# Kernel optimization log

Measured on AMD Instinct MI355X. Metric: run time of the kernel, lower is better.

## Reference

```python
import jax, jax.numpy as jnp
import numpy as np
from jax import lax

DIM = 128
HEADS = 8
B, H, W = 8, 128, 128


def conv1x1(w, x):
    # w: [out_c, in_c], x: [b, in_c, h, w]
    return jnp.einsum('oc,bchw->bohw', w, x)


def setup_inputs() -> dict:
    key = jax.random.key(0)
    ks = jax.random.split(key, 12)
    s = 0.02
    return {
        'x': jax.random.normal(ks[0], (B, DIM, H, W), dtype=jnp.float32),
        'W_qkv': jax.random.normal(ks[1], (3 * DIM, DIM), dtype=jnp.float32) * s,
        'W_dw': jax.random.normal(ks[2], (DIM, 1, 3, 3), dtype=jnp.float32) * s,
        'W_proj_s': jax.random.normal(ks[3], (DIM, DIM), dtype=jnp.float32) * s,
        'scale_s': jnp.ones((HEADS, 1, 1), dtype=jnp.float32),
        'W_ff1': jax.random.normal(ks[4], (DIM, DIM), dtype=jnp.float32) * s,
        'W_ff2': jax.random.normal(ks[5], (DIM, DIM), dtype=jnp.float32) * s,
        'W_proj_f': jax.random.normal(ks[6], (DIM, DIM), dtype=jnp.float32) * s,
        'W_gsf': jax.random.normal(ks[7], (DIM, DIM), dtype=jnp.float32) * s,
        'b_gsf': jnp.zeros((DIM,), dtype=jnp.float32),
        'W_gfs': jax.random.normal(ks[8], (DIM, DIM), dtype=jnp.float32) * s,
        'b_gfs': jnp.zeros((DIM,), dtype=jnp.float32),
    }


def reference(x, W_qkv, W_dw, W_proj_s, scale_s, W_ff1, W_ff2, W_proj_f,
              W_gsf, b_gsf, W_gfs, b_gfs):
    b, c, h, w = x.shape
    head = HEADS
    ch = c // head

    # --- channel self-attention branch ---
    qkv = conv1x1(W_qkv, x)                      # [b, 3c, h, w]
    q_s, k_s, v_s = jnp.split(qkv, 3, axis=1)
    v_s_conv = lax.conv_general_dilated(
        v_s, W_dw, window_strides=(1, 1), padding='SAME',
        feature_group_count=c,
        dimension_numbers=('NCHW', 'OIHW', 'NCHW'))  # depthwise 3x3

    q = q_s.reshape(b, head, ch, h * w)
    k = k_s.reshape(b, head, ch, h * w)
    v = v_s.reshape(b, head, ch, h * w)
    attn = jax.nn.softmax(jnp.einsum('bhcn,bhdn->bhcd', q, k) * scale_s, axis=-1)
    out_s = jnp.einsum('bhcd,bhdn->bhcn', attn, v).reshape(b, c, h, w)
    out_s = conv1x1(W_proj_s, out_s + v_s_conv)

    # --- frequency filter branch ---
    xf = jnp.fft.rfft2(x, norm='ortho')          # complex [b,c,h,w//2+1]
    spatial_weights = conv1x1(W_ff2, jax.nn.gelu(conv1x1(W_ff1, x), approximate=False))
    freq_weights = jnp.fft.rfft2(spatial_weights, norm='ortho')
    out_f = jnp.fft.irfft2(xf * freq_weights, s=(h, w), norm='ortho')
    out_f = conv1x1(W_proj_f, out_f)

    # --- sigmoid-gated fusion ---
    gate_f = jax.nn.sigmoid(conv1x1(W_gsf, out_s) + b_gsf[:, None, None])
    gate_s = jax.nn.sigmoid(conv1x1(W_gfs, out_f) + b_gfs[:, None, None])
    return x + out_s * gate_s + out_f * gate_f
```

## Files before the change

kernel.cpp:

```cpp
#include <hip/hip_runtime.h>
#include <math.h>

#define HW 16384

typedef __attribute__((ext_vector_type(8))) short bf16x8;
typedef __attribute__((ext_vector_type(4))) float f32x4;

__device__ __forceinline__ unsigned f2bf_pk(float a, float b)
{
    unsigned ua = __float_as_uint(a), ub = __float_as_uint(b);
    ua = (ua + 0x7FFFu + ((ua >> 16) & 1u)) >> 16;
    ub = (ub + 0x7FFFu + ((ub >> 16) & 1u)) >> 16;
    return (ua & 0xFFFFu) | (ub << 16);
}
__device__ __forceinline__ unsigned short f2bf(float a)
{
    unsigned ua = __float_as_uint(a);
    ua = (ua + 0x7FFFu + ((ua >> 16) & 1u)) >> 16;
    return (unsigned short)ua;
}
__device__ __forceinline__ float bf2f(unsigned short u)
{
    return __uint_as_float(((unsigned)u) << 16);
}
__device__ __forceinline__ float sigmoidf_(float v) { return 1.f / (1.f + expf(-v)); }

__device__ __forceinline__ float2 cmul(float2 a, float2 b)
{
    return make_float2(a.x * b.x - a.y * b.y, a.x * b.y + a.y * b.x);
}

__device__ __forceinline__ int SWZ2(int r, int j)
{
    return j ^ (r & 7) ^ ((((j >> 4) ^ (r >> 1)) & 1) << 3);
}

__global__ __launch_bounds__(256)
void wprep_k(const float* __restrict__ w0, const float* __restrict__ w1,
             const float* __restrict__ w2, const float* __restrict__ w3,
             const float* __restrict__ w4, const float* __restrict__ w5,
             const float* __restrict__ w6, int4* __restrict__ Wbf4)
{
    int m = blockIdx.x >> 3;
    int slot = (blockIdx.x & 7) * 256 + threadIdx.x;
    const float* src;
    switch (m) {
        case 0: src = w0; break;
        case 1: src = w1; break;
        case 2: src = w2; break;
        case 3: src = w3; break;
        case 4: src = w4; break;
        case 5: src = w5; break;
        default: src = w6; break;
    }
    int o = slot >> 4;
    int c16 = (slot & 15) ^ (o & 7);
    const float* p = src + o * 128 + c16 * 8;
    int4 pk;
    pk.x = f2bf_pk(p[0], p[1]); pk.y = f2bf_pk(p[2], p[3]);
    pk.z = f2bf_pk(p[4], p[5]); pk.w = f2bf_pk(p[6], p[7]);
    Wbf4[m * 2048 + slot] = pk;
}

__global__ __launch_bounds__(256)
void conv_mfma_k(const float* __restrict__ in, const int4* __restrict__ wbf,
                 unsigned short* __restrict__ out)
{
    __shared__ short WL[128 * 128];
    __shared__ short XL[64 * 128];
    int t = threadIdx.x;
    int gb = blockIdx.x;
    int b = gb >> 8;
    int n0 = (gb & 255) << 6;

    #pragma unroll
    for (int it = 0; it < 8; ++it)
        ((int4*)WL)[it * 256 + t] = wbf[it * 256 + t];

    const float* inb = in + (size_t)b * 128 * HW + n0;
    int nl = t & 63;
    #pragma unroll
    for (int it = 0; it < 4; ++it) {
        int c8 = (t >> 6) + it * 4;
        float v[8];
        #pragma unroll
        for (int j = 0; j < 8; ++j) v[j] = inb[(size_t)(c8 * 8 + j) * HW + nl];
        int4 p;
        p.x = f2bf_pk(v[0], v[1]); p.y = f2bf_pk(v[2], v[3]);
        p.z = f2bf_pk(v[4], v[5]); p.w = f2bf_pk(v[6], v[7]);
        ((int4*)XL)[nl * 16 + (c8 ^ (nl & 7))] = p;
    }
    __syncthreads();

    int l = t & 63, w = t >> 6, kg = l >> 4, l15 = l & 15, l7 = l15 & 7;
    f32x4 acc[2][4];
    #pragma unroll
    for (int mf = 0; mf < 2; ++mf)
        #pragma unroll
        for (int nf = 0; nf < 4; ++nf) acc[mf][nf] = (f32x4){0.f, 0.f, 0.f, 0.f};
    #pragma unroll
    for (int ks = 0; ks < 4; ++ks) {
        int ch = ks * 4 + kg;
        bf16x8 A0 = ((const bf16x8*)WL)[(w * 32 + l15) * 16 + (ch ^ l7)];
        bf16x8 A1 = ((const bf16x8*)WL)[(w * 32 + 16 + l15) * 16 + (ch ^ l7)];
        #pragma unroll
        for (int nf = 0; nf < 4; ++nf) {
            bf16x8 Bf = ((const bf16x8*)XL)[(nf * 16 + l15) * 16 + (ch ^ l7)];
            acc[0][nf] = __builtin_amdgcn_mfma_f32_16x16x32_bf16(A0, Bf, acc[0][nf], 0, 0, 0);
            acc[1][nf] = __builtin_amdgcn_mfma_f32_16x16x32_bf16(A1, Bf, acc[1][nf], 0, 0, 0);
        }
    }
    #pragma unroll
    for (int mf = 0; mf < 2; ++mf)
        #pragma unroll
        for (int nf = 0; nf < 4; ++nf)
            #pragma unroll
            for (int i = 0; i < 4; ++i) {
                int row = w * 32 + mf * 16 + kg * 4 + i;
                int col = n0 + nf * 16 + l15;
                out[((size_t)b * 128 + row) * HW + col] = f2bf(acc[mf][nf][i]);
            }
}

__global__ __launch_bounds__(256)
void conv_mfma_bf_k(const unsigned short* __restrict__ in,
                    const int4* __restrict__ wbf,
                    unsigned short* __restrict__ out)
{
    __shared__ short WL[128 * 128];
    __shared__ short XL[64 * 128];
    int t = threadIdx.x;
    int gb = blockIdx.x;
    int b = gb >> 8;
    int n0 = (gb & 255) << 6;

    #pragma unroll
    for (int it = 0; it < 8; ++it)
        ((int4*)WL)[it * 256 + t] = wbf[it * 256 + t];

    const unsigned short* inb = in + (size_t)b * 128 * HW + n0;
    int nl = t & 63;
    #pragma unroll
    for (int it = 0; it < 4; ++it) {
        int c8 = (t >> 6) + it * 4;
        unsigned u[8];
        #pragma unroll
        for (int j = 0; j < 8; ++j) u[j] = inb[(size_t)(c8 * 8 + j) * HW + nl];
        int4 p;
        p.x = (int)(u[0] | (u[1] << 16)); p.y = (int)(u[2] | (u[3] << 16));
        p.z = (int)(u[4] | (u[5] << 16)); p.w = (int)(u[6] | (u[7] << 16));
        ((int4*)XL)[nl * 16 + (c8 ^ (nl & 7))] = p;
    }
    __syncthreads();

    int l = t & 63, w = t >> 6, kg = l >> 4, l15 = l & 15, l7 = l15 & 7;
    f32x4 acc[2][4];
    #pragma unroll
    for (int mf = 0; mf < 2; ++mf)
        #pragma unroll
        for (int nf = 0; nf < 4; ++nf) acc[mf][nf] = (f32x4){0.f, 0.f, 0.f, 0.f};
    #pragma unroll
    for (int ks = 0; ks < 4; ++ks) {
        int ch = ks * 4 + kg;
        bf16x8 A0 = ((const bf16x8*)WL)[(w * 32 + l15) * 16 + (ch ^ l7)];
        bf16x8 A1 = ((const bf16x8*)WL)[(w * 32 + 16 + l15) * 16 + (ch ^ l7)];
        #pragma unroll
        for (int nf = 0; nf < 4; ++nf) {
            bf16x8 Bf = ((const bf16x8*)XL)[(nf * 16 + l15) * 16 + (ch ^ l7)];
            acc[0][nf] = __builtin_amdgcn_mfma_f32_16x16x32_bf16(A0, Bf, acc[0][nf], 0, 0, 0);
            acc[1][nf] = __builtin_amdgcn_mfma_f32_16x16x32_bf16(A1, Bf, acc[1][nf], 0, 0, 0);
        }
    }
    #pragma unroll
    for (int mf = 0; mf < 2; ++mf)
        #pragma unroll
        for (int nf = 0; nf < 4; ++nf)
            #pragma unroll
            for (int i = 0; i < 4; ++i) {
                int row = w * 32 + mf * 16 + kg * 4 + i;
                int col = n0 + nf * 16 + l15;
                out[((size_t)b * 128 + row) * HW + col] = f2bf(acc[mf][nf][i]);
            }
}

__global__ __launch_bounds__(256)
void dwconv_k(const unsigned short* __restrict__ V, const float* __restrict__ Wdw,
              unsigned short* __restrict__ vcb)
{
    int tid = blockIdx.x * 256 + threadIdx.x;
    int e4 = tid & 4095;
    int bc = tid >> 12;
    int c = bc & 127;
    int y = e4 >> 5;
    int x0 = (e4 & 31) << 2;
    const unsigned short* vin = V + (size_t)bc * HW;
    float wf[9];
    #pragma unroll
    for (int i = 0; i < 9; ++i) wf[i] = Wdw[c * 9 + i];
    float a0 = 0.f, a1 = 0.f, a2 = 0.f, a3 = 0.f;
    #pragma unroll
    for (int dy = 0; dy < 3; ++dy) {
        int yy = y + dy - 1;
        if (yy < 0 || yy > 127) continue;
        const unsigned short* r = vin + yy * 128;
        uint2 mu = *(const uint2*)(r + x0);
        float m0 = bf2f((unsigned short)(mu.x & 0xFFFF));
        float m1 = bf2f((unsigned short)(mu.x >> 16));
        float m2 = bf2f((unsigned short)(mu.y & 0xFFFF));
        float m3 = bf2f((unsigned short)(mu.y >> 16));
        float left  = (x0 > 0)   ? bf2f(r[x0 - 1]) : 0.f;
        float right = (x0 < 124) ? bf2f(r[x0 + 4]) : 0.f;
        float w0 = wf[dy * 3], w1 = wf[dy * 3 + 1], w2 = wf[dy * 3 + 2];
        a0 += w0 * left + w1 * m0 + w2 * m1;
        a1 += w0 * m0   + w1 * m1 + w2 * m2;
        a2 += w0 * m1   + w1 * m2 + w2 * m3;
        a3 += w0 * m2   + w1 * m3 + w2 * right;
    }
    uint2 r2;
    r2.x = f2bf_pk(a0, a1);
    r2.y = f2bf_pk(a2, a3);
    *(uint2*)(vcb + (size_t)bc * HW + y * 128 + x0) = r2;
}

__global__ __launch_bounds__(256)
void gram_mfma_k(const float* __restrict__ x, float* __restrict__ Gp)
{
    __shared__ short XL[128 * 128];
    int t = threadIdx.x;
    int blk = blockIdx.x;
    int b = blk >> 5, ks = blk & 31;
    const float* xb = x + (size_t)b * 128 * HW + ks * 512;
    int l = t & 63, w = t >> 6, kg = l >> 4, l15 = l & 15, l7 = l15 & 7;

    f32x4 acc[2][8];
    #pragma unroll
    for (int mf = 0; mf < 2; ++mf)
        #pragma unroll
        for (int nf = 0; nf < 8; ++nf) acc[mf][nf] = (f32x4){0.f, 0.f, 0.f, 0.f};

    for (int kc = 0; kc < 4; ++kc) {
        __syncthreads();
        #pragma unroll
        for (int it = 0; it < 8; ++it) {
            int g = it * 256 + t;
            int row = g >> 4, oct = g & 15;
            const float* p = xb + (size_t)row * HW + kc * 128 + oct * 8;
            int4 pk;
            pk.x = f2bf_pk(p[0], p[1]); pk.y = f2bf_pk(p[2], p[3]);
            pk.z = f2bf_pk(p[4], p[5]); pk.w = f2bf_pk(p[6], p[7]);
            ((int4*)XL)[row * 16 + (oct ^ (row & 7))] = pk;
        }
        __syncthreads();
        #pragma unroll
        for (int s = 0; s < 4; ++s) {
            int oct = s * 4 + kg;
            bf16x8 A0 = ((const bf16x8*)XL)[(w * 32 + l15) * 16 + (oct ^ l7)];
            bf16x8 A1 = ((const bf16x8*)XL)[(w * 32 + 16 + l15) * 16 + (oct ^ l7)];
            #pragma unroll
            for (int nf = 0; nf < 8; ++nf) {
                bf16x8 Bf = ((const bf16x8*)XL)[(nf * 16 + l15) * 16 + (oct ^ l7)];
                acc[0][nf] = __builtin_amdgcn_mfma_f32_16x16x32_bf16(A0, Bf, acc[0][nf], 0, 0, 0);
                acc[1][nf] = __builtin_amdgcn_mfma_f32_16x16x32_bf16(A1, Bf, acc[1][nf], 0, 0, 0);
            }
        }
    }
    float* gp = Gp + (size_t)blk * 16384;
    #pragma unroll
    for (int mf = 0; mf < 2; ++mf)
        #pragma unroll
        for (int nf = 0; nf < 8; ++nf)
            #pragma unroll
            for (int i = 0; i < 4; ++i) {
                int row = w * 32 + mf * 16 + kg * 4 + i;
                int col = nf * 16 + l15;
                gp[row * 128 + col] = acc[mf][nf][i];
            }
}

__global__ void gram_reduce_k(const float* __restrict__ Gp, float* __restrict__ G)
{
    int idx = blockIdx.x * 256 + threadIdx.x;
    int b = idx >> 14;
    int ij = idx & 16383;
    const float* gp = Gp + (size_t)(b * 32) * 16384 + ij;
    float s = 0.f;
    #pragma unroll
    for (int ks = 0; ks < 32; ++ks) s += gp[(size_t)ks * 16384];
    G[idx] = s;
}

__global__ __launch_bounds__(256)
void attn_s2_k(const float* __restrict__ G, const float* __restrict__ Wqkv,
               const float* __restrict__ scale, float* __restrict__ S)
{
    __shared__ float Wq[16][129];
    __shared__ float Wk[16][129];
    __shared__ float Ts[16][129];
    int bh = blockIdx.x;
    int b = bh >> 3, h = bh & 7;
    int t = threadIdx.x;
    #pragma unroll
    for (int i = 0; i < 8; ++i) {
        int idx = t + i * 256;
        int r = idx >> 7, ci = idx & 127;
        Wq[r][ci] = Wqkv[(size_t)(h * 16 + r) * 128 + ci];
        Wk[r][ci] = Wqkv[(size_t)(128 + h * 16 + r) * 128 + ci];
    }
    __syncthreads();
    const float* Gb = G + (size_t)b * 16384;
    #pragma unroll
    for (int i = 0; i < 8; ++i) {
        int idx = t + i * 256;
        int c = idx >> 7, col = idx & 127;
        float s = 0.f;
        #pragma unroll 8
        for (int ci = 0; ci < 128; ++ci)
            s += Wq[c][ci] * Gb[ci * 128 + col];
        Ts[c][col] = s;
    }
    __syncthreads();
    int c = t >> 4, d = t & 15;
    float s = 0.f;
    #pragma unroll 8
    for (int col = 0; col < 128; ++col)
        s += Ts[c][col] * Wk[d][col];
    s *= scale[h];
    float m = s;
    #pragma unroll
    for (int w = 1; w < 16; w <<= 1)
        m = fmaxf(m, __shfl_xor(m, w, 64));
    float e = expf(s - m);
    float sum = e;
    #pragma unroll
    for (int w = 1; w < 16; w <<= 1)
        sum += __shfl_xor(sum, w, 64);
    S[(size_t)bh * 256 + t] = e / sum;
}

__global__ __launch_bounds__(256)
void proj_s_pv_k(const unsigned short* __restrict__ V,
                 const unsigned short* __restrict__ vcb,
                 const float* __restrict__ S, const int4* __restrict__ wbf,
                 unsigned short* __restrict__ out_s)
{
    __shared__ short WL[128 * 128];
    __shared__ short XL[64 * 128];
    __shared__ float SL[2048];
    int t = threadIdx.x;
    int gb = blockIdx.x;
    int b = gb >> 8;
    int n0 = (gb & 255) << 6;

    #pragma unroll
    for (int it = 0; it < 8; ++it)
        ((int4*)WL)[it * 256 + t] = wbf[it * 256 + t];
    #pragma unroll
    for (int i = 0; i < 8; ++i)
        SL[i * 256 + t] = S[(size_t)b * 2048 + i * 256 + t];
    __syncthreads();

    int col = t & 63, w = t >> 6;
    #pragma unroll
    for (int hh = 0; hh < 2; ++hh) {
        int h = w * 2 + hh;
        float v[16];
        #pragma unroll
        for (int d = 0; d < 16; ++d)
            v[d] = bf2f(V[((size_t)(b * 128 + h * 16 + d)) * HW + n0 + col]);
        float o[16];
        #pragma unroll
        for (int c = 0; c < 16; ++c) {
            const float* sl = SL + h * 256 + c * 16;
            float s = 0.f;
            #pragma unroll
            for (int d = 0; d < 16; ++d) s += sl[d] * v[d];
            o[c] = s + bf2f(vcb[((size_t)(b * 128 + h * 16 + c)) * HW + n0 + col]);
        }
        #pragma unroll
        for (int oc = 0; oc < 2; ++oc) {
            int octet = h * 2 + oc;
            int4 p;
            p.x = f2bf_pk(o[oc * 8 + 0], o[oc * 8 + 1]);
            p.y = f2bf_pk(o[oc * 8 + 2], o[oc * 8 + 3]);
            p.z = f2bf_pk(o[oc * 8 + 4], o[oc * 8 + 5]);
            p.w = f2bf_pk(o[oc * 8 + 6], o[oc * 8 + 7]);
            ((int4*)XL)[col * 16 + (octet ^ (col & 7))] = p;
        }
    }
    __syncthreads();

    int l = t & 63, kg = l >> 4, l15 = l & 15, l7 = l15 & 7;
    f32x4 acc[2][4];
    #pragma unroll
    for (int mf = 0; mf < 2; ++mf)
        #pragma unroll
        for (int nf = 0; nf < 4; ++nf) acc[mf][nf] = (f32x4){0.f, 0.f, 0.f, 0.f};
    #pragma unroll
    for (int ks = 0; ks < 4; ++ks) {
        int ch = ks * 4 + kg;
        bf16x8 A0 = ((const bf16x8*)WL)[(w * 32 + l15) * 16 + (ch ^ l7)];
        bf16x8 A1 = ((const bf16x8*)WL)[(w * 32 + 16 + l15) * 16 + (ch ^ l7)];
        #pragma unroll
        for (int nf = 0; nf < 4; ++nf) {
            bf16x8 Bf = ((const bf16x8*)XL)[(nf * 16 + l15) * 16 + (ch ^ l7)];
            acc[0][nf] = __builtin_amdgcn_mfma_f32_16x16x32_bf16(A0, Bf, acc[0][nf], 0, 0, 0);
            acc[1][nf] = __builtin_amdgcn_mfma_f32_16x16x32_bf16(A1, Bf, acc[1][nf], 0, 0, 0);
        }
    }
    #pragma unroll
    for (int mf = 0; mf < 2; ++mf)
        #pragma unroll
        for (int nf = 0; nf < 4; ++nf)
            #pragma unroll
            for (int i = 0; i < 4; ++i) {
                int row = w * 32 + mf * 16 + kg * 4 + i;
                int colg = n0 + nf * 16 + l15;
                out_s[((size_t)b * 128 + row) * HW + colg] = f2bf(acc[mf][nf][i]);
            }
}

__global__ __launch_bounds__(256)
void ff_fused_k(const float* __restrict__ x, const int4* __restrict__ w1bf,
                const int4* __restrict__ w2bf, unsigned short* __restrict__ outp)
{
    __shared__ short WL[128 * 128];
    __shared__ short XL[64 * 128];
    int t = threadIdx.x;
    int gb = blockIdx.x;
    int b = gb >> 8;
    int n0 = (gb & 255) << 6;

    #pragma unroll
    for (int it = 0; it < 8; ++it)
        ((int4*)WL)[it * 256 + t] = w1bf[it * 256 + t];

    const float* inb = x + (size_t)b * 128 * HW + n0;
    int nl = t & 63;
    #pragma unroll
    for (int it = 0; it < 4; ++it) {
        int c8 = (t >> 6) + it * 4;
        float v[8];
        #pragma unroll
        for (int j = 0; j < 8; ++j) v[j] = inb[(size_t)(c8 * 8 + j) * HW + nl];
        int4 p;
        p.x = f2bf_pk(v[0], v[1]); p.y = f2bf_pk(v[2], v[3]);
        p.z = f2bf_pk(v[4], v[5]); p.w = f2bf_pk(v[6], v[7]);
        ((int4*)XL)[nl * 16 + (c8 ^ (nl & 7))] = p;
    }
    __syncthreads();

    int l = t & 63, w = t >> 6, kg = l >> 4, l15 = l & 15, l7 = l15 & 7;
    f32x4 acc[2][4];
    #pragma unroll
    for (int mf = 0; mf < 2; ++mf)
        #pragma unroll
        for (int nf = 0; nf < 4; ++nf) acc[mf][nf] = (f32x4){0.f, 0.f, 0.f, 0.f};
    #pragma unroll
    for (int ks = 0; ks < 4; ++ks) {
        int ch = ks * 4 + kg;
        bf16x8 A0 = ((const bf16x8*)WL)[(w * 32 + l15) * 16 + (ch ^ l7)];
        bf16x8 A1 = ((const bf16x8*)WL)[(w * 32 + 16 + l15) * 16 + (ch ^ l7)];
        #pragma unroll
        for (int nf = 0; nf < 4; ++nf) {
            bf16x8 Bf = ((const bf16x8*)XL)[(nf * 16 + l15) * 16 + (ch ^ l7)];
            acc[0][nf] = __builtin_amdgcn_mfma_f32_16x16x32_bf16(A0, Bf, acc[0][nf], 0, 0, 0);
            acc[1][nf] = __builtin_amdgcn_mfma_f32_16x16x32_bf16(A1, Bf, acc[1][nf], 0, 0, 0);
        }
    }
    __syncthreads();

    #pragma unroll
    for (int it = 0; it < 8; ++it)
        ((int4*)WL)[it * 256 + t] = w2bf[it * 256 + t];
    #pragma unroll
    for (int mf = 0; mf < 2; ++mf)
        #pragma unroll
        for (int nf = 0; nf < 4; ++nf) {
            float g4[4];
            #pragma unroll
            for (int i = 0; i < 4; ++i) {
                float v = acc[mf][nf][i];
                g4[i] = 0.5f * v * (1.0f + erff(v * 0.70710678118654752f));
            }
            int col = nf * 16 + l15;
            int r0 = w * 32 + mf * 16 + kg * 4;
            int octet = r0 >> 3;
            uint2 pk2;
            pk2.x = f2bf_pk(g4[0], g4[1]);
            pk2.y = f2bf_pk(g4[2], g4[3]);
            ((uint2*)XL)[(col * 16 + (octet ^ (col & 7))) * 2 + (kg & 1)] = pk2;
        }
    __syncthreads();

    f32x4 acc2[2][4];
    #pragma unroll
    for (int mf = 0; mf < 2; ++mf)
        #pragma unroll
        for (int nf = 0; nf < 4; ++nf) acc2[mf][nf] = (f32x4){0.f, 0.f, 0.f, 0.f};
    #pragma unroll
    for (int ks = 0; ks < 4; ++ks) {
        int ch = ks * 4 + kg;
        bf16x8 A0 = ((const bf16x8*)WL)[(w * 32 + l15) * 16 + (ch ^ l7)];
        bf16x8 A1 = ((const bf16x8*)WL)[(w * 32 + 16 + l15) * 16 + (ch ^ l7)];
        #pragma unroll
        for (int nf = 0; nf < 4; ++nf) {
            bf16x8 Bf = ((const bf16x8*)XL)[(nf * 16 + l15) * 16 + (ch ^ l7)];
            acc2[0][nf] = __builtin_amdgcn_mfma_f32_16x16x32_bf16(A0, Bf, acc2[0][nf], 0, 0, 0);
            acc2[1][nf] = __builtin_amdgcn_mfma_f32_16x16x32_bf16(A1, Bf, acc2[1][nf], 0, 0, 0);
        }
    }
    #pragma unroll
    for (int mf = 0; mf < 2; ++mf)
        #pragma unroll
        for (int nf = 0; nf < 4; ++nf)
            #pragma unroll
            for (int i = 0; i < 4; ++i) {
                int row = w * 32 + mf * 16 + kg * 4 + i;
                int col = n0 + nf * 16 + l15;
                outp[((size_t)b * 128 + row) * HW + col] = f2bf(acc2[mf][nf][i]);
            }
}

__global__ __launch_bounds__(256)
void fuse2_k(const float* __restrict__ x, const unsigned short* __restrict__ outs,
             const unsigned short* __restrict__ outf,
             const int4* __restrict__ wgsf_bf, const float* __restrict__ bgsf,
             const int4* __restrict__ wgfs_bf, const float* __restrict__ bgfs,
             float* __restrict__ out)
{
    __shared__ short WS[64 * 128];
    __shared__ short WF[64 * 128];
    __shared__ short XS[64 * 128];
    __shared__ short XF[64 * 128];
    int t = threadIdx.x;
    int gb = blockIdx.x;
    int half = gb & 1;
    int nt = (gb >> 1) & 255;
    int b = gb >> 9;
    int n0 = nt << 6;

    #pragma unroll
    for (int it = 0; it < 4; ++it) {
        ((int4*)WS)[it * 256 + t] = wgsf_bf[half * 1024 + it * 256 + t];
        ((int4*)WF)[it * 256 + t] = wgfs_bf[half * 1024 + it * 256 + t];
    }
    const unsigned short* sb = outs + (size_t)b * 128 * HW + n0;
    const unsigned short* fb = outf + (size_t)b * 128 * HW + n0;
    int nl = t & 63;
    #pragma unroll
    for (int it = 0; it < 4; ++it) {
        int c8 = (t >> 6) + it * 4;
        unsigned us[8], uf[8];
        #pragma unroll
        for (int j = 0; j < 8; ++j) {
            size_t a = (size_t)(c8 * 8 + j) * HW + nl;
            us[j] = sb[a];
            uf[j] = fb[a];
        }
        int4 ps, pf;
        ps.x = (int)(us[0] | (us[1] << 16)); ps.y = (int)(us[2] | (us[3] << 16));
        ps.z = (int)(us[4] | (us[5] << 16)); ps.w = (int)(us[6] | (us[7] << 16));
        pf.x = (int)(uf[0] | (uf[1] << 16)); pf.y = (int)(uf[2] | (uf[3] << 16));
        pf.z = (int)(uf[4] | (uf[5] << 16)); pf.w = (int)(uf[6] | (uf[7] << 16));
        ((int4*)XS)[nl * 16 + (c8 ^ (nl & 7))] = ps;
        ((int4*)XF)[nl * 16 + (c8 ^ (nl & 7))] = pf;
    }
    __syncthreads();

    int l = t & 63, w = t >> 6, kg = l >> 4, l15 = l & 15, l7 = l15 & 7;
    f32x4 aS[4], aF[4];
    #pragma unroll
    for (int nf = 0; nf < 4; ++nf) {
        aS[nf] = (f32x4){0.f, 0.f, 0.f, 0.f};
        aF[nf] = (f32x4){0.f, 0.f, 0.f, 0.f};
    }
    #pragma unroll
    for (int ks = 0; ks < 4; ++ks) {
        int ch = ks * 4 + kg;
        bf16x8 As = ((const bf16x8*)WS)[(w * 16 + l15) * 16 + (ch ^ l7)];
        bf16x8 Af = ((const bf16x8*)WF)[(w * 16 + l15) * 16 + (ch ^ l7)];
        #pragma unroll
        for (int nf = 0; nf < 4; ++nf) {
            bf16x8 Bs = ((const bf16x8*)XS)[(nf * 16 + l15) * 16 + (ch ^ l7)];
            bf16x8 Bf = ((const bf16x8*)XF)[(nf * 16 + l15) * 16 + (ch ^ l7)];
            aS[nf] = __builtin_amdgcn_mfma_f32_16x16x32_bf16(As, Bs, aS[nf], 0, 0, 0);
            aF[nf] = __builtin_amdgcn_mfma_f32_16x16x32_bf16(Af, Bf, aF[nf], 0, 0, 0);
        }
    }
    #pragma unroll
    for (int nf = 0; nf < 4; ++nf)
        #pragma unroll
        for (int i = 0; i < 4; ++i) {
            int row = half * 64 + w * 16 + kg * 4 + i;
            int cc = nf * 16 + l15;
            float gf = sigmoidf_(aS[nf][i] + bgsf[row]);
            float gs = sigmoidf_(aF[nf][i] + bgfs[row]);
            size_t gi = ((size_t)(b * 128) + row) * HW + n0 + cc;
            float os = bf2f(outs[gi]);
            float of = bf2f(outf[gi]);
            out[gi] = x[gi] + os * gs + of * gf;
        }
}

__device__ __forceinline__ void dft16(float2* v)
{
    const float C1 = 0.92387953251f, S1 = 0.38268343236f, R2 = 0.70710678119f;
    const float2 W16[8] = {
        {1.f, 0.f}, {C1, -S1}, {R2, -R2}, {S1, -C1},
        {0.f, -1.f}, {-S1, -C1}, {-R2, -R2}, {-C1, -S1}};
    #pragma unroll
    for (int i = 0; i < 8; ++i) {
        float2 a = v[i], b = v[i + 8];
        v[i] = make_float2(a.x + b.x, a.y + b.y);
        float2 d = make_float2(a.x - b.x, a.y - b.y);
        v[i + 8] = cmul(d, W16[i]);
    }
    #pragma unroll
    for (int blk = 0; blk < 16; blk += 8)
        #pragma unroll
        for (int i = 0; i < 4; ++i) {
            float2 a = v[blk + i], b = v[blk + i + 4];
            v[blk + i] = make_float2(a.x + b.x, a.y + b.y);
            float2 d = make_float2(a.x - b.x, a.y - b.y);
            v[blk + i + 4] = cmul(d, W16[2 * i]);
        }
    #pragma unroll
    for (int blk = 0; blk < 16; blk += 4) {
        float2 a0 = v[blk], b0 = v[blk + 2];
        v[blk] = make_float2(a0.x + b0.x, a0.y + b0.y);
        v[blk + 2] = make_float2(a0.x - b0.x, a0.y - b0.y);
        float2 a1 = v[blk + 1], b1 = v[blk + 3];
        v[blk + 1] = make_float2(a1.x + b1.x, a1.y + b1.y);
        float2 d = make_float2(a1.x - b1.x, a1.y - b1.y);
        v[blk + 3] = make_float2(d.y, -d.x);
    }
    #pragma unroll
    for (int blk = 0; blk < 16; blk += 2) {
        float2 a = v[blk], b = v[blk + 1];
        v[blk] = make_float2(a.x + b.x, a.y + b.y);
        v[blk + 1] = make_float2(a.x - b.x, a.y - b.y);
    }
}

__device__ __forceinline__ void dft8(float2* v)
{
    const float R2 = 0.70710678119f;
    const float2 W8[4] = {{1.f, 0.f}, {R2, -R2}, {0.f, -1.f}, {-R2, -R2}};
    #pragma unroll
    for (int i = 0; i < 4; ++i) {
        float2 a = v[i], b = v[i + 4];
        v[i] = make_float2(a.x + b.x, a.y + b.y);
        float2 d = make_float2(a.x - b.x, a.y - b.y);
        v[i + 4] = cmul(d, W8[i]);
    }
    #pragma unroll
    for (int blk = 0; blk < 8; blk += 4) {
        float2 a0 = v[blk], b0 = v[blk + 2];
        v[blk] = make_float2(a0.x + b0.x, a0.y + b0.y);
        v[blk + 2] = make_float2(a0.x - b0.x, a0.y - b0.y);
        float2 a1 = v[blk + 1], b1 = v[blk + 3];
        v[blk + 1] = make_float2(a1.x + b1.x, a1.y + b1.y);
        float2 d = make_float2(a1.x - b1.x, a1.y - b1.y);
        v[blk + 3] = make_float2(d.y, -d.x);
    }
    #pragma unroll
    for (int blk = 0; blk < 8; blk += 2) {
        float2 a = v[blk], b = v[blk + 1];
        v[blk] = make_float2(a.x + b.x, a.y + b.y);
        v[blk + 1] = make_float2(a.x - b.x, a.y - b.y);
    }
}

__device__ __forceinline__ void fwd128(float2 (*buf)[128], const float2* tw,
                                       int row, int n2, bool cj,
                                       float2* wa, float2* wb)
{
    const int BREV4[16] = {0,8,4,12,2,10,6,14,1,9,5,13,3,11,7,15};
    float2 v[16];
    #pragma unroll
    for (int n1 = 0; n1 < 16; ++n1) {
        float2 a = buf[row][SWZ2(row, 8 * n1 + n2)];
        v[n1] = cj ? make_float2(a.x, -a.y) : a;
    }
    dft16(v);
    __syncthreads();
    #pragma unroll
    for (int p = 0; p < 16; ++p) {
        int k1 = BREV4[p];
        buf[row][SWZ2(row, 16 * n2 + k1)] = cmul(v[p], tw[n2 * k1]);
    }
    __syncthreads();
    #pragma unroll
    for (int m = 0; m < 8; ++m) wa[m] = buf[row][SWZ2(row, 16 * m + n2)];
    #pragma unroll
    for (int m = 0; m < 8; ++m) wb[m] = buf[row][SWZ2(row, 16 * m + n2 + 8)];
    dft8(wa);
    dft8(wb);
}

__device__ __forceinline__ int rowL(int g, int i)
{
    if (g == 0) {
        if (i < 16) return i;
        if (i < 31) return 127 - (i - 16);
        return 64;
    }
    return (i < 16) ? (16 * g + i) : (128 - (16 * g + (i - 16)));
}

__global__ __launch_bounds__(256)
void fft_p1_k(const float* __restrict__ x, const unsigned short* __restrict__ sw,
              unsigned* __restrict__ A)
{
    __shared__ float2 buf[32][128];
    __shared__ float2 tw[128];
    const int BREV3[8] = {0,4,2,6,1,5,3,7};
    int t = threadIdx.x;
    if (t < 128) {
        float sn, cs;
        sincosf(0.049087385212340519f * (float)t, &sn, &cs);
        tw[t] = make_float2(cs, -sn);
    }
    int ch = blockIdx.x >> 2;
    int rg = blockIdx.x & 3;
    size_t base = (size_t)ch * HW + rg * 4096;
    #pragma unroll
    for (int i = 0; i < 16; ++i) {
        int idx = t + i * 256;
        int r = idx >> 7, cc = idx & 127;
        buf[r][SWZ2(r, cc)] = make_float2(x[base + r * 128 + cc],
                                          bf2f(sw[base + r * 128 + cc]));
    }
    __syncthreads();
    int row = t >> 3, n2 = t & 7;
    float2 wa[8], wb[8];
    fwd128(buf, tw, row, n2, false, wa, wb);
    size_t cb = (size_t)ch * HW + rg * 32 + row;
    #pragma unroll
    for (int p = 0; p < 8; ++p) {
        int ka = n2 + 16 * BREV3[p];
        int kb = n2 + 8 + 16 * BREV3[p];
        A[cb + (size_t)ka * 128] = f2bf_pk(wa[p].x, wa[p].y);
        A[cb + (size_t)kb * 128] = f2bf_pk(wb[p].x, wb[p].y);
    }
}

__global__ __launch_bounds__(256)
void fft_p234_k(unsigned* __restrict__ A)
{
    __shared__ float2 buf[32][128];
    __shared__ float2 tw[128];
    const int BREV3[8] = {0,4,2,6,1,5,3,7};
    int t = threadIdx.x;
    if (t < 128) {
        float sn, cs;
        sincosf(0.049087385212340519f * (float)t, &sn, &cs);
        tw[t] = make_float2(cs, -sn);
    }
    int ch = blockIdx.x >> 2;
    int g = blockIdx.x & 3;
    size_t cb = (size_t)ch * HW;

    #pragma unroll
    for (int i = 0; i < 16; ++i) {
        int idx = t + i * 256;
        int r = idx >> 7, cc = idx & 127;
        unsigned z = A[cb + (size_t)rowL(g, r) * 128 + cc];
        buf[r][SWZ2(r, cc)] = make_float2(bf2f((unsigned short)(z & 0xFFFF)),
                                          bf2f((unsigned short)(z >> 16)));
    }
    __syncthreads();
    int row = t >> 3, n2 = t & 7;
    float2 wa[8], wb[8];
    fwd128(buf, tw, row, n2, false, wa, wb);
    __syncthreads();
    #pragma unroll
    for (int p = 0; p < 8; ++p) {
        buf[row][SWZ2(row, n2 + 16 * BREV3[p])] = wa[p];
        buf[row][SWZ2(row, n2 + 8 + 16 * BREV3[p])] = wb[p];
    }
    __syncthreads();

    int nItems = (g == 0) ? 2050 : 2048;
    for (int item = t; item < nItems; item += 256) {
        int rA, rB, k2;
        if (g == 0) {
            if (item < 1920)      { int j = item >> 7; rA = 1 + j; rB = 16 + j; k2 = item & 127; }
            else if (item < 1985) { rA = rB = 0;  k2 = item - 1920; }
            else                  { rA = rB = 31; k2 = item - 1985; }
        } else {
            int j = item >> 7; rA = j; rB = 16 + j; k2 = item & 127;
        }
        int pk2 = (128 - k2) & 127;
        int pA = SWZ2(rA, k2), pB = SWZ2(rB, pk2);
        float2 z1 = buf[rA][pA];
        float2 z2 = buf[rB][pB];
        float2 X = make_float2(0.5f * (z1.x + z2.x), 0.5f * (z1.y - z2.y));
        float Dx = z1.x - z2.x, Dy = z1.y + z2.y;
        float2 Wf = make_float2(0.5f * Dy, -0.5f * Dx);
        float2 Y = cmul(X, Wf);
        buf[rA][pA] = Y;
        buf[rB][pB] = make_float2(Y.x, -Y.y);
    }
    __syncthreads();

    fwd128(buf, tw, row, n2, true, wa, wb);
    size_t rb = cb + (size_t)rowL(g, row) * 128;
    #pragma unroll
    for (int p = 0; p < 8; ++p) {
        int ka = n2 + 16 * BREV3[p];
        int kb = n2 + 8 + 16 * BREV3[p];
        A[rb + ka] = f2bf_pk(wa[p].x, -wa[p].y);
        A[rb + kb] = f2bf_pk(wb[p].x, -wb[p].y);
    }
}

__global__ __launch_bounds__(256)
void fft_p5_k(const unsigned* __restrict__ A, unsigned short* __restrict__ outp)
{
    __shared__ float2 buf[32][128];
    __shared__ float2 tw[128];
    const int BREV3[8] = {0,4,2,6,1,5,3,7};
    int t = threadIdx.x;
    if (t < 128) {
        float sn, cs;
        sincosf(0.049087385212340519f * (float)t, &sn, &cs);
        tw[t] = make_float2(cs, -sn);
    }
    int ch = blockIdx.x >> 2;
    int rg = blockIdx.x & 3;
    size_t cb = (size_t)ch * HW;
    int rbase = rg * 32;
    #pragma unroll
    for (int i = 0; i < 16; ++i) {
        int idx = t + i * 256;
        int rl = idx & 31, kw = idx >> 5;
        unsigned z = A[cb + (size_t)kw * 128 + rbase + rl];
        buf[rl][SWZ2(rl, kw)] = make_float2(bf2f((unsigned short)(z & 0xFFFF)),
                                            -bf2f((unsigned short)(z >> 16)));
    }
    __syncthreads();
    int row = t >> 3, n2 = t & 7;
    float2 wa[8], wb[8];
    fwd128(buf, tw, row, n2, false, wa, wb);
    const float scale = 1.f / 2097152.f;
    size_t ob = cb + (size_t)(rbase + row) * 128;
    #pragma unroll
    for (int p = 0; p < 8; ++p) {
        int ka = n2 + 16 * BREV3[p];
        int kb = n2 + 8 + 16 * BREV3[p];
        outp[ob + ka] = f2bf(wa[p].x * scale);
        outp[ob + kb] = f2bf(wb[p].x * scale);
    }
}

extern "C" void kernel_launch(void* const* d_in, const int* in_sizes, int n_in,
                              void* d_out, int out_size, void* d_ws, size_t ws_size,
                              hipStream_t stream)
{
    const float* x        = (const float*)d_in[0];
    const float* W_qkv    = (const float*)d_in[1];
    const float* W_dw     = (const float*)d_in[2];
    const float* W_proj_s = (const float*)d_in[3];
    const float* scale_s  = (const float*)d_in[4];
    const float* W_ff1    = (const float*)d_in[5];
    const float* W_ff2    = (const float*)d_in[6];
    const float* W_proj_f = (const float*)d_in[7];
    const float* W_gsf    = (const float*)d_in[8];
    const float* b_gsf    = (const float*)d_in[9];
    const float* W_gfs    = (const float*)d_in[10];
    const float* b_gfs    = (const float*)d_in[11];
    float* out = (float*)d_out;

    char* ws = (char*)d_ws;
    const size_t MB32 = 33554432ull;
    const size_t MB64 = 67108864ull;
    const size_t MB96 = 100663296ull;
    unsigned short* V     = (unsigned short*)(ws);
    unsigned short* out_s = (unsigned short*)(ws + MB32);
    unsigned short* swb   = (unsigned short*)(ws + MB64);
    unsigned short* pre   = (unsigned short*)(ws + MB64);
    unsigned short* out_fp= (unsigned short*)(ws);
    int4* Wbf4            = (int4*)(ws + MB96);
    unsigned short* vcb   = (unsigned short*)out;
    float* Gp  = out + 8388608;
    float* G   = out + 8388608 + 4194304;
    float* S   = G + 131072;
    unsigned* A = (unsigned*)out;

    wprep_k<<<56, 256, 0, stream>>>(W_qkv + 256 * 128, W_proj_s, W_ff1, W_ff2,
                                    W_proj_f, W_gsf, W_gfs, Wbf4);

    conv_mfma_k<<<2048, 256, 0, stream>>>(x, Wbf4 + 0 * 2048, V);
    dwconv_k<<<16384, 256, 0, stream>>>(V, W_dw, vcb);
    gram_mfma_k<<<256, 256, 0, stream>>>(x, Gp);
    gram_reduce_k<<<512, 256, 0, stream>>>(Gp, G);
    attn_s2_k<<<64, 256, 0, stream>>>(G, W_qkv, scale_s, S);
    proj_s_pv_k<<<2048, 256, 0, stream>>>(V, vcb, S, Wbf4 + 1 * 2048, out_s);

    ff_fused_k<<<2048, 256, 0, stream>>>(x, Wbf4 + 2 * 2048, Wbf4 + 3 * 2048, swb);
    fft_p1_k<<<4096, 256, 0, stream>>>(x, swb, A);
    fft_p234_k<<<4096, 256, 0, stream>>>(A);
    fft_p5_k<<<4096, 256, 0, stream>>>(A, pre);
    conv_mfma_bf_k<<<2048, 256, 0, stream>>>(pre, Wbf4 + 4 * 2048, out_fp);

    fuse2_k<<<4096, 256, 0, stream>>>(x, out_s, out_fp,
                                      Wbf4 + 5 * 2048, b_gsf,
                                      Wbf4 + 6 * 2048, b_gfs, out);
}
```

Measured before the change: 349.4 us.

## Fuse three FFT kernels into one per-channel kernel with full-image LDS tile

```diff
diff --git a/kernel.cpp b/kernel.cpp
--- a/kernel.cpp
+++ b/kernel.cpp
@@ -28,11 +28,6 @@
 __device__ __forceinline__ float2 cmul(float2 a, float2 b)
 {
     return make_float2(a.x * b.x - a.y * b.y, a.x * b.y + a.y * b.x);
-}
-
-__device__ __forceinline__ int SWZ2(int r, int j)
-{
-    return j ^ (r & 7) ^ ((((j >> 4) ^ (r >> 1)) & 1) << 3);
 }
 
 __global__ __launch_bounds__(256)
@@ -602,6 +597,21 @@
         }
 }
 
+__device__ __forceinline__ int ZIX(int r, int j)
+{
+    return r * 128 + (j ^ ((r & 3) << 3) ^ (((j >> 4) & 3) << 1));
+}
+__device__ __forceinline__ float2 zld(const unsigned* Z, int r, int j)
+{
+    unsigned z = Z[ZIX(r, j)];
+    return make_float2(bf2f((unsigned short)(z & 0xFFFF)),
+                       bf2f((unsigned short)(z >> 16)));
+}
+__device__ __forceinline__ void zst(unsigned* Z, int r, int j, float2 v)
+{
+    Z[ZIX(r, j)] = f2bf_pk(v.x, v.y);
+}
+
 __device__ __forceinline__ void dft16(float2* v)
 {
     const float C1 = 0.92387953251f, S1 = 0.38268343236f, R2 = 0.70710678119f;
@@ -671,48 +681,69 @@
     }
 }
 
-__device__ __forceinline__ void fwd128(float2 (*buf)[128], const float2* tw,
-                                       int row, int n2, bool cj,
-                                       float2* wa, float2* wb)
+__device__ __forceinline__ void fft_line_row(unsigned* Z, const float2* tw,
+                                             int row, int n2)
 {
     const int BREV4[16] = {0,8,4,12,2,10,6,14,1,9,5,13,3,11,7,15};
+    const int BREV3[8] = {0,4,2,6,1,5,3,7};
     float2 v[16];
     #pragma unroll
-    for (int n1 = 0; n1 < 16; ++n1) {
-        float2 a = buf[row][SWZ2(row, 8 * n1 + n2)];
-        v[n1] = cj ? make_float2(a.x, -a.y) : a;
-    }
+    for (int n1 = 0; n1 < 16; ++n1) v[n1] = zld(Z, row, 8 * n1 + n2);
     dft16(v);
-    __syncthreads();
     #pragma unroll
     for (int p = 0; p < 16; ++p) {
         int k1 = BREV4[p];
-        buf[row][SWZ2(row, 16 * n2 + k1)] = cmul(v[p], tw[n2 * k1]);
-    }
-    __syncthreads();
-    #pragma unroll
-    for (int m = 0; m < 8; ++m) wa[m] = buf[row][SWZ2(row, 16 * m + n2)];
-    #pragma unroll
-    for (int m = 0; m < 8; ++m) wb[m] = buf[row][SWZ2(row, 16 * m + n2 + 8)];
+        zst(Z, row, 16 * n2 + k1, cmul(v[p], tw[n2 * k1]));
+    }
+    float2 wa[8], wb[8];
+    #pragma unroll
+    for (int m = 0; m < 8; ++m) {
+        wa[m] = zld(Z, row, 16 * m + n2);
+        wb[m] = zld(Z, row, 16 * m + n2 + 8);
+    }
     dft8(wa);
     dft8(wb);
-}
-
-__device__ __forceinline__ int rowL(int g, int i)
-{
-    if (g == 0) {
-        if (i < 16) return i;
-        if (i < 31) return 127 - (i - 16);
-        return 64;
-    }
-    return (i < 16) ? (16 * g + i) : (128 - (16 * g + (i - 16)));
-}
-
-__global__ __launch_bounds__(256)
-void fft_p1_k(const float* __restrict__ x, const unsigned short* __restrict__ sw,
-              unsigned* __restrict__ A)
-{
-    __shared__ float2 buf[32][128];
+    #pragma unroll
+    for (int p = 0; p < 8; ++p) {
+        zst(Z, row, n2 + 16 * BREV3[p], wa[p]);
+        zst(Z, row, n2 + 8 + 16 * BREV3[p], wb[p]);
+    }
+}
+
+__device__ __forceinline__ void fft_line_col(unsigned* Z, const float2* tw,
+                                             int col, int n2)
+{
+    const int BREV4[16] = {0,8,4,12,2,10,6,14,1,9,5,13,3,11,7,15};
+    const int BREV3[8] = {0,4,2,6,1,5,3,7};
+    float2 v[16];
+    #pragma unroll
+    for (int n1 = 0; n1 < 16; ++n1) v[n1] = zld(Z, 8 * n1 + n2, col);
+    dft16(v);
+    #pragma unroll
+    for (int p = 0; p < 16; ++p) {
+        int k1 = BREV4[p];
+        zst(Z, 16 * n2 + k1, col, cmul(v[p], tw[n2 * k1]));
+    }
+    float2 wa[8], wb[8];
+    #pragma unroll
+    for (int m = 0; m < 8; ++m) {
+        wa[m] = zld(Z, 16 * m + n2, col);
+        wb[m] = zld(Z, 16 * m + n2 + 8, col);
+    }
+    dft8(wa);
+    dft8(wb);
+    #pragma unroll
+    for (int p = 0; p < 8; ++p) {
+        zst(Z, n2 + 16 * BREV3[p], col, wa[p]);
+        zst(Z, n2 + 8 + 16 * BREV3[p], col, wb[p]);
+    }
+}
+
+__global__ __launch_bounds__(256)
+void fft_all_k(const float* __restrict__ x, const unsigned short* __restrict__ sw,
+               unsigned short* __restrict__ outp)
+{
+    __shared__ unsigned Z[128 * 128];
     __shared__ float2 tw[128];
     const int BREV3[8] = {0,4,2,6,1,5,3,7};
     int t = threadIdx.x;
@@ -721,136 +752,76 @@
         sincosf(0.049087385212340519f * (float)t, &sn, &cs);
         tw[t] = make_float2(cs, -sn);
     }
-    int ch = blockIdx.x >> 2;
-    int rg = blockIdx.x & 3;
-    size_t base = (size_t)ch * HW + rg * 4096;
-    #pragma unroll
-    for (int i = 0; i < 16; ++i) {
+    size_t base = (size_t)blockIdx.x * HW;
+
+    for (int i = 0; i < 64; ++i) {
         int idx = t + i * 256;
-        int r = idx >> 7, cc = idx & 127;
-        buf[r][SWZ2(r, cc)] = make_float2(x[base + r * 128 + cc],
-                                          bf2f(sw[base + r * 128 + cc]));
-    }
-    __syncthreads();
-    int row = t >> 3, n2 = t & 7;
-    float2 wa[8], wb[8];
-    fwd128(buf, tw, row, n2, false, wa, wb);
-    size_t cb = (size_t)ch * HW + rg * 32 + row;
-    #pragma unroll
-    for (int p = 0; p < 8; ++p) {
-        int ka = n2 + 16 * BREV3[p];
-        int kb = n2 + 8 + 16 * BREV3[p];
-        A[cb + (size_t)ka * 128] = f2bf_pk(wa[p].x, wa[p].y);
-        A[cb + (size_t)kb * 128] = f2bf_pk(wb[p].x, wb[p].y);
-    }
-}
-
-__global__ __launch_bounds__(256)
-void fft_p234_k(unsigned* __restrict__ A)
-{
-    __shared__ float2 buf[32][128];
-    __shared__ float2 tw[128];
-    const int BREV3[8] = {0,4,2,6,1,5,3,7};
-    int t = threadIdx.x;
-    if (t < 128) {
-        float sn, cs;
-        sincosf(0.049087385212340519f * (float)t, &sn, &cs);
-        tw[t] = make_float2(cs, -sn);
-    }
-    int ch = blockIdx.x >> 2;
-    int g = blockIdx.x & 3;
-    size_t cb = (size_t)ch * HW;
-
-    #pragma unroll
-    for (int i = 0; i < 16; ++i) {
-        int idx = t + i * 256;
-        int r = idx >> 7, cc = idx & 127;
-        unsigned z = A[cb + (size_t)rowL(g, r) * 128 + cc];
-        buf[r][SWZ2(r, cc)] = make_float2(bf2f((unsigned short)(z & 0xFFFF)),
-                                          bf2f((unsigned short)(z >> 16)));
-    }
-    __syncthreads();
-    int row = t >> 3, n2 = t & 7;
-    float2 wa[8], wb[8];
-    fwd128(buf, tw, row, n2, false, wa, wb);
-    __syncthreads();
-    #pragma unroll
-    for (int p = 0; p < 8; ++p) {
-        buf[row][SWZ2(row, n2 + 16 * BREV3[p])] = wa[p];
-        buf[row][SWZ2(row, n2 + 8 + 16 * BREV3[p])] = wb[p];
-    }
-    __syncthreads();
-
-    int nItems = (g == 0) ? 2050 : 2048;
-    for (int item = t; item < nItems; item += 256) {
-        int rA, rB, k2;
-        if (g == 0) {
-            if (item < 1920)      { int j = item >> 7; rA = 1 + j; rB = 16 + j; k2 = item & 127; }
-            else if (item < 1985) { rA = rB = 0;  k2 = item - 1920; }
-            else                  { rA = rB = 31; k2 = item - 1985; }
+        int r = idx >> 7, j = idx & 127;
+        Z[ZIX(r, j)] = f2bf_pk(x[base + idx], bf2f(sw[base + idx]));
+    }
+    __syncthreads();
+
+    int ln = t >> 3, n2 = t & 7;
+    #pragma unroll
+    for (int it = 0; it < 4; ++it) fft_line_row(Z, tw, it * 32 + ln, n2);
+    __syncthreads();
+    #pragma unroll
+    for (int it = 0; it < 4; ++it) fft_line_col(Z, tw, it * 32 + ln, n2);
+    __syncthreads();
+
+    for (int item = t; item < 8194; item += 256) {
+        int rA, kA, rB, kB;
+        if (item < 8064) {
+            rA = 1 + (item >> 7); kA = item & 127;
+            rB = 128 - rA; kB = (128 - kA) & 127;
         } else {
-            int j = item >> 7; rA = j; rB = 16 + j; k2 = item & 127;
-        }
-        int pk2 = (128 - k2) & 127;
-        int pA = SWZ2(rA, k2), pB = SWZ2(rB, pk2);
-        float2 z1 = buf[rA][pA];
-        float2 z2 = buf[rB][pB];
+            int it2 = item - 8064;
+            rA = rB = (it2 < 65) ? 0 : 64;
+            kA = (it2 < 65) ? it2 : (it2 - 65);
+            kB = (128 - kA) & 127;
+        }
+        float2 z1 = zld(Z, rA, kA);
+        float2 z2 = zld(Z, rB, kB);
         float2 X = make_float2(0.5f * (z1.x + z2.x), 0.5f * (z1.y - z2.y));
         float Dx = z1.x - z2.x, Dy = z1.y + z2.y;
         float2 Wf = make_float2(0.5f * Dy, -0.5f * Dx);
         float2 Y = cmul(X, Wf);
-        buf[rA][pA] = Y;
-        buf[rB][pB] = make_float2(Y.x, -Y.y);
-    }
-    __syncthreads();
-
-    fwd128(buf, tw, row, n2, true, wa, wb);
-    size_t rb = cb + (size_t)rowL(g, row) * 128;
-    #pragma unroll
-    for (int p = 0; p < 8; ++p) {
-        int ka = n2 + 16 * BREV3[p];
-        int kb = n2 + 8 + 16 * BREV3[p];
-        A[rb + ka] = f2bf_pk(wa[p].x, -wa[p].y);
-        A[rb + kb] = f2bf_pk(wb[p].x, -wb[p].y);
-    }
-}
-
-__global__ __launch_bounds__(256)
-void fft_p5_k(const unsigned* __restrict__ A, unsigned short* __restrict__ outp)
-{
-    __shared__ float2 buf[32][128];
-    __shared__ float2 tw[128];
-    const int BREV3[8] = {0,4,2,6,1,5,3,7};
-    int t = threadIdx.x;
-    if (t < 128) {
-        float sn, cs;
-        sincosf(0.049087385212340519f * (float)t, &sn, &cs);
-        tw[t] = make_float2(cs, -sn);
-    }
-    int ch = blockIdx.x >> 2;
-    int rg = blockIdx.x & 3;
-    size_t cb = (size_t)ch * HW;
-    int rbase = rg * 32;
-    #pragma unroll
-    for (int i = 0; i < 16; ++i) {
-        int idx = t + i * 256;
-        int rl = idx & 31, kw = idx >> 5;
-        unsigned z = A[cb + (size_t)kw * 128 + rbase + rl];
-        buf[rl][SWZ2(rl, kw)] = make_float2(bf2f((unsigned short)(z & 0xFFFF)),
-                                            -bf2f((unsigned short)(z >> 16)));
-    }
-    __syncthreads();
-    int row = t >> 3, n2 = t & 7;
-    float2 wa[8], wb[8];
-    fwd128(buf, tw, row, n2, false, wa, wb);
+        zst(Z, rA, kA, make_float2(Y.x, -Y.y));
+        zst(Z, rB, kB, Y);
+    }
+    __syncthreads();
+
+    #pragma unroll
+    for (int it = 0; it < 4; ++it) fft_line_col(Z, tw, it * 32 + ln, n2);
+    __syncthreads();
+
     const float scale = 1.f / 2097152.f;
-    size_t ob = cb + (size_t)(rbase + row) * 128;
-    #pragma unroll
-    for (int p = 0; p < 8; ++p) {
-        int ka = n2 + 16 * BREV3[p];
-        int kb = n2 + 8 + 16 * BREV3[p];
-        outp[ob + ka] = f2bf(wa[p].x * scale);
-        outp[ob + kb] = f2bf(wb[p].x * scale);
+    const int BREV4[16] = {0,8,4,12,2,10,6,14,1,9,5,13,3,11,7,15};
+    #pragma unroll
+    for (int it = 0; it < 4; ++it) {
+        int row = it * 32 + ln;
+        float2 v[16];
+        #pragma unroll
+        for (int n1 = 0; n1 < 16; ++n1) v[n1] = zld(Z, row, 8 * n1 + n2);
+        dft16(v);
+        #pragma unroll
+        for (int p = 0; p < 16; ++p) {
+            int k1 = BREV4[p];
+            zst(Z, row, 16 * n2 + k1, cmul(v[p], tw[n2 * k1]));
+        }
+        float2 wa[8], wb[8];
+        #pragma unroll
+        for (int m = 0; m < 8; ++m) {
+            wa[m] = zld(Z, row, 16 * m + n2);
+            wb[m] = zld(Z, row, 16 * m + n2 + 8);
+        }
+        dft8(wa);
+        dft8(wb);
+        #pragma unroll
+        for (int p = 0; p < 8; ++p) {
+            outp[base + row * 128 + n2 + 16 * BREV3[p]] = f2bf(wa[p].x * scale);
+            outp[base + row * 128 + n2 + 8 + 16 * BREV3[p]] = f2bf(wb[p].x * scale);
+        }
     }
 }
 
@@ -886,7 +857,6 @@
     float* Gp  = out + 8388608;
     float* G   = out + 8388608 + 4194304;
     float* S   = G + 131072;
-    unsigned* A = (unsigned*)out;
 
     wprep_k<<<56, 256, 0, stream>>>(W_qkv + 256 * 128, W_proj_s, W_ff1, W_ff2,
                                     W_proj_f, W_gsf, W_gfs, Wbf4);
@@ -899,9 +869,7 @@
     proj_s_pv_k<<<2048, 256, 0, stream>>>(V, vcb, S, Wbf4 + 1 * 2048, out_s);
 
     ff_fused_k<<<2048, 256, 0, stream>>>(x, Wbf4 + 2 * 2048, Wbf4 + 3 * 2048, swb);
-    fft_p1_k<<<4096, 256, 0, stream>>>(x, swb, A);
-    fft_p234_k<<<4096, 256, 0, stream>>>(A);
-    fft_p5_k<<<4096, 256, 0, stream>>>(A, pre);
+    fft_all_k<<<1024, 256, 0, stream>>>(x, swb, pre);
     conv_mfma_bf_k<<<2048, 256, 0, stream>>>(pre, Wbf4 + 4 * 2048, out_fp);
 
     fuse2_k<<<4096, 256, 0, stream>>>(x, out_s, out_fp,
```

Measured after the change: 330.5 us. 5.4% less time.
